# Kernel tuning notes

Measured on AMD Instinct MI355X. Metric: run time of the kernel, lower is better.

The kernel has to match this reference:

```python
import jax, jax.numpy as jnp
import numpy as np

VOCAB = 50257
EMBED = 128
B, S = 64, 4096


def setup_inputs() -> dict:
    key = jax.random.key(0)
    k1, k2, k3 = jax.random.split(key, 3)
    x = jax.random.randint(k1, (B, S), 0, VOCAB)
    # Linear(n_symboles, output_size) weight has shape [output_size, n_symboles]
    W = jax.random.normal(k2, (EMBED, VOCAB), dtype=jnp.float32) * 0.02
    b = jax.random.normal(k3, (EMBED,), dtype=jnp.float32) * 0.02
    return {"x": x, "W": W, "b": b}


def reference(x, W, b):
    # one_hot(x, V) @ W.T + b  ==  gather rows of W.T at x, then add bias.
    # Mathematically identical to the torch one-hot + Linear path, but
    # avoids materializing the [B, S, V] one-hot tensor.
    return W.T[x] + b  # [B, S, EMBED]
```

## Files before the change

kernel.cpp:

```cpp
#include <hip/hip_runtime.h>

#define VOCAB 50257
#define EMBED 128
#define NTOK  (64 * 4096)
#define NSLICE 8

typedef float    f32x4 __attribute__((ext_vector_type(4)));
typedef _Float16 f16x4 __attribute__((ext_vector_type(4)));
typedef _Float16 f16x8 __attribute__((ext_vector_type(8)));

__global__ void transpose_h_kernel(const float* __restrict__ W,
                                   const float* __restrict__ bias,
                                   _Float16* __restrict__ Wt) {
    __shared__ float tile[64][65];
    const int t  = threadIdx.x;
    const int v0 = blockIdx.x * 64;
    const int e0 = blockIdx.y * 64;
    const bool full = (v0 + 64 <= VOCAB);

    if (full) {
#pragma unroll
        for (int it = 0; it < 4; ++it) {
            const int e_loc = (t >> 4) + it * 16;
            const int c4    = (t & 15) * 4;
            f32x4 val = *(const f32x4*)&W[(size_t)(e0 + e_loc) * VOCAB + v0 + c4];
            tile[c4 + 0][e_loc] = val.x;
            tile[c4 + 1][e_loc] = val.y;
            tile[c4 + 2][e_loc] = val.z;
            tile[c4 + 3][e_loc] = val.w;
        }
    } else {
#pragma unroll
        for (int it = 0; it < 16; ++it) {
            const int e_loc = (t >> 6) + it * 4;
            const int c     = t & 63;
            const int v     = v0 + c;
            tile[c][e_loc] = (v < VOCAB) ? W[(size_t)(e0 + e_loc) * VOCAB + v]
                                         : 0.0f;
        }
    }
    __syncthreads();

    const int eo = (t & 7) * 8;
    const int eg = e0 + eo;
    const int s  = eg >> 4;
    const int ep = eg & 15;
    const f32x4 ba = *(const f32x4*)&bias[eg];
    const f32x4 bb = *(const f32x4*)&bias[eg + 4];
#pragma unroll
    for (int it = 0; it < 2; ++it) {
        const int v_loc = (t >> 3) + it * 32;
        const int v     = v0 + v_loc;
        if (v < VOCAB) {
            f16x8 h;
            h[0] = (_Float16)(tile[v_loc][eo + 0] + ba.x);
            h[1] = (_Float16)(tile[v_loc][eo + 1] + ba.y);
            h[2] = (_Float16)(tile[v_loc][eo + 2] + ba.z);
            h[3] = (_Float16)(tile[v_loc][eo + 3] + ba.w);
            h[4] = (_Float16)(tile[v_loc][eo + 4] + bb.x);
            h[5] = (_Float16)(tile[v_loc][eo + 5] + bb.y);
            h[6] = (_Float16)(tile[v_loc][eo + 6] + bb.z);
            h[7] = (_Float16)(tile[v_loc][eo + 7] + bb.w);
            *(f16x8*)&Wt[((size_t)s * VOCAB + v) * 16 + ep] = h;
        }
    }
}

__global__ void gather_sliced_kernel(const int* __restrict__ x,
                                     const f16x4* __restrict__ Wt,
                                     f32x4* __restrict__ out) {
    const int bid   = blockIdx.x;
    const int slice = bid & (NSLICE - 1);
    const int tblk  = bid >> 3;
    const int t     = threadIdx.x;
    const int tok   = tblk * 64 + (t >> 2);
    const int q     = t & 3;
    const int idx   = x[tok];
    const f16x4 h = Wt[((size_t)slice * VOCAB + idx) * 4 + q];
    f32x4 r;
    r.x = (float)h[0];
    r.y = (float)h[1];
    r.z = (float)h[2];
    r.w = (float)h[3];
    out[(size_t)tok * 32 + slice * 4 + q] = r;
}

__global__ void direct_kernel(const int* __restrict__ x,
                              const float* __restrict__ W,
                              const float* __restrict__ bias,
                              f32x4* __restrict__ out) {
    const int gid   = blockIdx.x * blockDim.x + threadIdx.x;
    const int token = gid >> 5;
    const int e4    = gid & 31;
    const int idx   = x[token];
    const int e     = e4 * 4;
    f32x4 r;
    r.x = W[(size_t)(e + 0) * VOCAB + idx] + bias[e + 0];
    r.y = W[(size_t)(e + 1) * VOCAB + idx] + bias[e + 1];
    r.z = W[(size_t)(e + 2) * VOCAB + idx] + bias[e + 2];
    r.w = W[(size_t)(e + 3) * VOCAB + idx] + bias[e + 3];
    out[(size_t)token * 32 + e4] = r;
}

extern "C" void kernel_launch(void* const* d_in, const int* in_sizes, int n_in,
                              void* d_out, int out_size, void* d_ws, size_t ws_size,
                              hipStream_t stream) {
    const int*   x    = (const int*)d_in[0];
    const float* W    = (const float*)d_in[1];
    const float* bias = (const float*)d_in[2];

    const size_t wt_bytes = (size_t)VOCAB * EMBED * sizeof(_Float16);

    if (ws_size >= wt_bytes) {
        _Float16* Wt = (_Float16*)d_ws;
        dim3 tgrid((VOCAB + 63) / 64, 2);
        transpose_h_kernel<<<tgrid, 256, 0, stream>>>(W, bias, Wt);

        const int gblocks = (NTOK / 64) * NSLICE;
        gather_sliced_kernel<<<gblocks, 256, 0, stream>>>(x, (const f16x4*)Wt,
                                                          (f32x4*)d_out);
    } else {
        const int dblocks = (NTOK * 32) / 256;
        direct_kernel<<<dblocks, 256, 0, stream>>>(x, W, bias, (f32x4*)d_out);
    }
}
```

Baseline: 45.72 us.

## Fuse transpose and gather into one persistent cooperative kernel with grid sync

Merges the weight transpose/fp16-convert pass and the sliced gather into a single persistent cooperative kernel. Blocks first loop over transpose tiles, meet at a grid-wide barrier, then loop over gather work. The aim is to remove the second kernel launch and the gap between the two launches. In exchange it adds a host occupancy query and a grid sync, and caps the grid at 2048 persistent blocks, which may cut latency hiding in the gather phase.

Measured after the change: 152.9 us. +234.5%, slower.

```diff
diff --git a/kernel.cpp b/kernel.cpp
--- a/kernel.cpp
+++ b/kernel.cpp
@@ -1,13 +1,107 @@
 #include <hip/hip_runtime.h>
+#include <hip/hip_cooperative_groups.h>
+
+namespace cg = cooperative_groups;
 
 #define VOCAB 50257
 #define EMBED 128
 #define NTOK  (64 * 4096)
 #define NSLICE 8
+#define NBLK  (NTOK / 64)
+#define NVB   (NBLK * NSLICE)
+#define NTILE_V 786
+#define NTILE (NTILE_V * 2)
+#define NCU   256
 
 typedef float    f32x4 __attribute__((ext_vector_type(4)));
 typedef _Float16 f16x4 __attribute__((ext_vector_type(4)));
 typedef _Float16 f16x8 __attribute__((ext_vector_type(8)));
+
+__global__ void __launch_bounds__(256, 8)
+fused_kernel(const int* __restrict__ x,
+             const float* __restrict__ W,
+             const float* __restrict__ bias,
+             _Float16* __restrict__ Wt,
+             f32x4* __restrict__ out) {
+    __shared__ float tile[64][65];
+    const int t    = threadIdx.x;
+    const int bid  = blockIdx.x;
+    const int grid = gridDim.x;
+
+    for (int tl = bid; tl < NTILE; tl += grid) {
+        const int v0 = (tl % NTILE_V) * 64;
+        const int e0 = (tl / NTILE_V) * 64;
+        const bool full = (v0 + 64 <= VOCAB);
+
+        if (full) {
+#pragma unroll
+            for (int it = 0; it < 4; ++it) {
+                const int e_loc = (t >> 4) + it * 16;
+                const int c4    = (t & 15) * 4;
+                f32x4 val = *(const f32x4*)&W[(size_t)(e0 + e_loc) * VOCAB + v0 + c4];
+                tile[c4 + 0][e_loc] = val.x;
+                tile[c4 + 1][e_loc] = val.y;
+                tile[c4 + 2][e_loc] = val.z;
+                tile[c4 + 3][e_loc] = val.w;
+            }
+        } else {
+#pragma unroll
+            for (int it = 0; it < 16; ++it) {
+                const int e_loc = (t >> 6) + it * 4;
+                const int c     = t & 63;
+                const int v     = v0 + c;
+                tile[c][e_loc] = (v < VOCAB) ? W[(size_t)(e0 + e_loc) * VOCAB + v]
+                                             : 0.0f;
+            }
+        }
+        __syncthreads();
+
+        const int eo = (t & 7) * 8;
+        const int eg = e0 + eo;
+        const int s  = eg >> 4;
+        const int ep = eg & 15;
+        const f32x4 ba = *(const f32x4*)&bias[eg];
+        const f32x4 bb = *(const f32x4*)&bias[eg + 4];
+#pragma unroll
+        for (int it = 0; it < 2; ++it) {
+            const int v_loc = (t >> 3) + it * 32;
+            const int v     = v0 + v_loc;
+            if (v < VOCAB) {
+                f16x8 h;
+                h[0] = (_Float16)(tile[v_loc][eo + 0] + ba.x);
+                h[1] = (_Float16)(tile[v_loc][eo + 1] + ba.y);
+                h[2] = (_Float16)(tile[v_loc][eo + 2] + ba.z);
+                h[3] = (_Float16)(tile[v_loc][eo + 3] + ba.w);
+                h[4] = (_Float16)(tile[v_loc][eo + 4] + bb.x);
+                h[5] = (_Float16)(tile[v_loc][eo + 5] + bb.y);
+                h[6] = (_Float16)(tile[v_loc][eo + 6] + bb.z);
+                h[7] = (_Float16)(tile[v_loc][eo + 7] + bb.w);
+                *(f16x8*)&Wt[((size_t)s * VOCAB + v) * 16 + ep] = h;
+            }
+        }
+        __syncthreads();
+    }
+
+    cg::this_grid().sync();
+
+    const int slice = bid & (NSLICE - 1);
+    const int lq    = t & 3;
+    const int lt    = t >> 2;
+    const f16x4* Wts = (const f16x4*)Wt + (size_t)slice * VOCAB * 4;
+
+    for (int vb = bid; vb < NVB; vb += grid) {
+        const int tblk = vb >> 3;
+        const int tok  = tblk * 64 + lt;
+        const int idx  = x[tok];
+        const f16x4 h  = Wts[(size_t)idx * 4 + lq];
+        f32x4 r;
+        r.x = (float)h[0];
+        r.y = (float)h[1];
+        r.z = (float)h[2];
+        r.w = (float)h[3];
+        out[(size_t)tok * 32 + slice * 4 + lq] = r;
+    }
+}
 
 __global__ void transpose_h_kernel(const float* __restrict__ W,
                                    const float* __restrict__ bias,
@@ -111,16 +205,30 @@
 
     const size_t wt_bytes = (size_t)VOCAB * EMBED * sizeof(_Float16);
 
-    if (ws_size >= wt_bytes) {
-        _Float16* Wt = (_Float16*)d_ws;
-        dim3 tgrid((VOCAB + 63) / 64, 2);
-        transpose_h_kernel<<<tgrid, 256, 0, stream>>>(W, bias, Wt);
-
-        const int gblocks = (NTOK / 64) * NSLICE;
-        gather_sliced_kernel<<<gblocks, 256, 0, stream>>>(x, (const f16x4*)Wt,
-                                                          (f32x4*)d_out);
-    } else {
+    if (ws_size < wt_bytes) {
         const int dblocks = (NTOK * 32) / 256;
         direct_kernel<<<dblocks, 256, 0, stream>>>(x, W, bias, (f32x4*)d_out);
-    }
-}
+        return;
+    }
+
+    _Float16* Wt = (_Float16*)d_ws;
+    f32x4*    o  = (f32x4*)d_out;
+
+    int blocks_per_cu = 0;
+    hipError_t qerr = hipOccupancyMaxActiveBlocksPerMultiprocessor(
+        &blocks_per_cu, (const void*)fused_kernel, 256, 0);
+
+    if (qerr == hipSuccess && blocks_per_cu >= 1) {
+        int grid = blocks_per_cu * NCU;
+        if (grid > 2048) grid = 2048;
+        void* args[] = {(void*)&x, (void*)&W, (void*)&bias, (void*)&Wt, (void*)&o};
+        hipError_t lerr = hipLaunchCooperativeKernel(
+            (const void*)fused_kernel, dim3(grid), dim3(256), args, 0, stream);
+        if (lerr == hipSuccess) return;
+    }
+
+    dim3 tgrid((VOCAB + 63) / 64, 2);
+    transpose_h_kernel<<<tgrid, 256, 0, stream>>>(W, bias, Wt);
+    const int gblocks = (NTOK / 64) * NSLICE;
+    gather_sliced_kernel<<<gblocks, 256, 0, stream>>>(x, (const f16x4*)Wt, o);
+}
```
